# Kernel tuning notes

Measured on AMD Instinct MI355X. Metric: run time of the kernel, lower is better.

## Reference

```python
import jax, jax.numpy as jnp
import numpy as np

B, T, K, H = 8, 1024, 128, 8
TOP_K = 64
KS = 5  # conv kernel size for Q/K
DN = ('NCH', 'OIH', 'NCH')


def setup_inputs() -> dict:
    key = jax.random.key(0)
    ks = jax.random.split(key, 9)
    s = 0.05
    return {
        'x': jax.random.normal(ks[0], (B, T, K), jnp.float32),
        'Wq': jax.random.normal(ks[1], (K * H, K, KS), jnp.float32) * s,
        'bq': jax.random.normal(ks[2], (K * H,), jnp.float32) * s,
        'Wk': jax.random.normal(ks[3], (K * H, K, KS), jnp.float32) * s,
        'bk': jax.random.normal(ks[4], (K * H,), jnp.float32) * s,
        'Wv': jax.random.normal(ks[5], (K * H, K, 1), jnp.float32) * s,
        'bv': jax.random.normal(ks[6], (K * H,), jnp.float32) * s,
        'Wu': jax.random.normal(ks[7], (K, K * H), jnp.float32) * s,
        'bu': jax.random.normal(ks[8], (K,), jnp.float32) * s,
    }


def _prep(z, b, k, h, t, scale):
    # z: (b, k*h, t) conv output; torch view(b,k,h,t) then transposes -> (b,h,t,k)
    z = z.reshape(b, k, h, t)
    z = jnp.transpose(z, (0, 2, 3, 1)) * scale  # (b, h, t, k)
    # torch: transpose(1,2).contiguous().view(b*h, t, k) -- replicate exactly
    z = jnp.transpose(z, (0, 2, 1, 3)).reshape(b * h, t, k)
    return z


def reference(x, Wq, bq, Wk, bk, Wv, bv, Wu, bu):
    b, t, k = x.shape
    h = H
    xc = jnp.transpose(x, (0, 2, 1))  # (b, k, t)
    # causal left-pad KS-1 for Q/K convs; V is pointwise (kernel 1)
    q = jax.lax.conv_general_dilated(xc, Wq, (1,), [(KS - 1, 0)], dimension_numbers=DN) + bq[None, :, None]
    kk = jax.lax.conv_general_dilated(xc, Wk, (1,), [(KS - 1, 0)], dimension_numbers=DN) + bk[None, :, None]
    v = jax.lax.conv_general_dilated(xc, Wv, (1,), [(0, 0)], dimension_numbers=DN) + bv[None, :, None]
    scale = k ** -0.25
    q = _prep(q, b, k, h, t, scale)
    kk = _prep(kk, b, k, h, t, scale)
    v = _prep(v, b, k, h, t, 1.0)
    w = jnp.einsum('btk,bsk->bts', q, kk)  # (b*h, t, t)
    # top-k sparsification: keep entries >= k-th largest per row, else row min
    largest, _ = jax.lax.top_k(w, TOP_K)
    thresh = jnp.min(largest, axis=-1, keepdims=True)
    row_min = jnp.min(w, axis=-1, keepdims=True)
    w = jnp.where(w >= thresh, w, row_min)
    # causal mask (strict upper triangle -> -inf)
    causal = jnp.triu(jnp.ones((t, t), bool), 1)
    w = jnp.where(causal[None], -jnp.inf, w)
    w = jax.nn.softmax(w, axis=-1)
    out = jnp.einsum('bts,bsk->btk', w, v)  # (b*h, t, k)
    out = out.reshape(b, h, t, k)
    out = jnp.transpose(out, (0, 2, 1, 3)).reshape(b, t, k * h)
    return out @ Wu.T + bu
```

## Files before the change

### kernel.cpp

```cpp
#include <hip/hip_runtime.h>
#include <hip/hip_fp16.h>
#include <cstdint>

using f16 = _Float16;
typedef __attribute__((ext_vector_type(8))) _Float16 f16x8;
typedef __attribute__((ext_vector_type(4))) _Float16 f16x4;
typedef __attribute__((ext_vector_type(4))) float f32x4;

#define MFMA16(a, b, c) __builtin_amdgcn_mfma_f32_16x16x32_f16((a), (b), (c), 0, 0, 0)

__device__ __forceinline__ f16x8 ldfrag(const f16* p) { return *(const f16x8*)p; }

__device__ __forceinline__ void dma16(const f16* g, f16* l) {
  __builtin_amdgcn_global_load_lds(
      (const __attribute__((address_space(1))) void*)g,
      (__attribute__((address_space(3))) void*)l, 16, 0, 0);
}
__device__ __forceinline__ void wait_vm0() {
  asm volatile("s_waitcnt vmcnt(0)" ::: "memory");
}
__device__ __forceinline__ void wait_lgkm0() {
  asm volatile("s_waitcnt lgkmcnt(0)" ::: "memory");
}
__device__ __forceinline__ void wait_vm4() {
  asm volatile("s_waitcnt vmcnt(4)" ::: "memory");
}
__device__ __forceinline__ void wait_vm2() {
  asm volatile("s_waitcnt vmcnt(2)" ::: "memory");
}

static const int64_t NX = 1048576;
static const int64_t NW = 655360;
static const int64_t NV = 131072;

__global__ __launch_bounds__(256) void k0_prep(
    const float* __restrict__ x, const float* __restrict__ Wq,
    const float* __restrict__ Wk, const float* __restrict__ Wv,
    const float* __restrict__ Wu,
    f16* __restrict__ xh, f16* __restrict__ xl,
    f16* __restrict__ Wqh, f16* __restrict__ Wql,
    f16* __restrict__ Wkh, f16* __restrict__ Wkl,
    f16* __restrict__ Wvb, f16* __restrict__ Wub) {
  int64_t i = (int64_t)blockIdx.x * 256 + threadIdx.x;
  if (i < NX) {
    const float v = x[i];
    const f16 h = (f16)v;
    xh[i] = h; xl[i] = (f16)(v - (float)h);
  } else if (i < NX + NW) {
    int64_t d = i - NX;
    int j = (int)(d >> 17);
    int rem = (int)(d & 131071);
    int o = rem >> 7, c = rem & 127;
    const float v = Wq[(int64_t)(o * 128 + c) * 5 + j];
    const f16 h = (f16)v;
    Wqh[d] = h; Wql[d] = (f16)(v - (float)h);
  } else if (i < NX + 2 * NW) {
    int64_t d = i - NX - NW;
    int j = (int)(d >> 17);
    int rem = (int)(d & 131071);
    int o = rem >> 7, c = rem & 127;
    const float v = Wk[(int64_t)(o * 128 + c) * 5 + j];
    const f16 h = (f16)v;
    Wkh[d] = h; Wkl[d] = (f16)(v - (float)h);
  } else if (i < NX + 2 * NW + NV) {
    int64_t d = i - NX - 2 * NW;
    Wvb[d] = (f16)Wv[d];
  } else {
    int64_t d = i - NX - 2 * NW - NV;
    Wub[d] = (f16)Wu[d];
  }
}

#define STAGE_QK(DST, PASS, VALEXPR)                                    \
  {                                                                     \
    __syncthreads();                                                    \
    _Pragma("unroll")                                                   \
    for (int nt = 0; nt < 8; ++nt) {                                    \
      const int o = o0 + nt * 16 + lo;                                  \
      const int kcl = (o >> 3) & 63, hh = o & 7;                        \
      _Pragma("unroll")                                                 \
      for (int rtl = 0; rtl < 2; ++rtl) {                               \
        const int rt = (PASS) * 2 + rtl;                                \
        _Pragma("unroll")                                               \
        for (int r = 0; r < 4; ++r) {                                   \
          const int t2l = (rtl * 16 + quad * 4 + r) * 8 + hh;           \
          lds[t2l * 72 + kcl] = (VALEXPR);                              \
        }                                                               \
      }                                                                 \
    }                                                                   \
    __syncthreads();                                                    \
    _Pragma("unroll")                                                   \
    for (int p = 0; p < 8; ++p) {                                       \
      const int idx = p * 256 + tid;                                    \
      const int a = idx >> 3, c8 = (idx & 7) * 8;                       \
      *(f16x8*)(DST + ((int64_t)m * 1024 + t2b + (PASS) * 256 + a) * 128 + \
                half * 64 + c8) = *(const f16x8*)&lds[a * 72 + c8];     \
    }                                                                   \
  }

__global__ __launch_bounds__(256) void k1_conv(
    const f16* __restrict__ xh, const f16* __restrict__ xl,
    const f16* __restrict__ Wqh, const f16* __restrict__ Wql,
    const f16* __restrict__ Wkh, const f16* __restrict__ Wkl,
    const f16* __restrict__ Wvb,
    const float* __restrict__ bq, const float* __restrict__ bk,
    const float* __restrict__ bv,
    f16* __restrict__ q3h, f16* __restrict__ q3l,
    f16* __restrict__ k3h, f16* __restrict__ k3l,
    f16* __restrict__ v3T) {
  __shared__ f16 shm[36384];
  f16* const wbuf = shm;
  f16* const xbuf = shm + 18432;
  f16* const lds  = shm;
  const int tid = threadIdx.x;
  const int w = tid >> 6, lane = tid & 63;
  const int quad = lane >> 4, lo = lane & 15;
  const int r0 = blockIdx.x * 64;
  const int bb = r0 >> 10;
  const int m  = r0 >> 7;
  const int t2b = (r0 & 127) * 8;
  const int tloc = r0 & 1023;
  const int half = blockIdx.y;
  const int isK = blockIdx.z;
  const int o0 = half * 512 + w * 128;

  const f16* Wh = isK ? Wkh : Wqh;
  const f16* Wl = isK ? Wkl : Wql;
  const float* bias = isK ? bk : bq;

#pragma unroll
  for (int p = 0; p < 9; ++p) {
    const int u = p * 256 + tid;
    if (u < 2176) {
      const int row = u >> 5, tz = (u >> 4) & 1, c8 = (u & 15) * 8;
      int lt = tloc - 4 + row;
      if (lt < 0) lt = 0;
      const f16* src = (tz ? xl : xh) + ((int64_t)(bb * 1024 + lt)) * 128 + c8;
      *(f16x8*)&xbuf[row * 264 + tz * 128 + c8] = *(const f16x8*)src;
    }
  }
  __syncthreads();

  const int64_t wlane = (int64_t)(lane & 15) * 128 + (lane >> 4) * 8;

  if (!isK) {
    f32x4 av[4][8];
#pragma unroll
    for (int rt = 0; rt < 4; ++rt)
#pragma unroll
      for (int i = 0; i < 8; ++i)
#pragma unroll
        for (int r = 0; r < 4; ++r) av[rt][i][r] = 0.f;

#pragma unroll
    for (int g = 0; g < 4; ++g) {
#pragma unroll
      for (int s = 0; s < 2; ++s) {
        const int64_t vsrc = (int64_t)(o0 + (g * 2 + s) * 16) * 128 + wlane;
#pragma unroll
        for (int kk = 0; kk < 4; ++kk)
          dma16(Wvb + vsrc + kk * 32, wbuf + w * 4096 + s * 2048 + kk * 512);
      }
      wait_vm0();
#pragma unroll
      for (int kk = 0; kk < 4; ++kk) {
        f16x8 a[4];
#pragma unroll
        for (int rt = 0; rt < 4; ++rt)
          a[rt] = *(const f16x8*)&xbuf[(rt * 16 + lo + 4) * 264 + kk * 32 +
                                       quad * 8];
#pragma unroll
        for (int s = 0; s < 2; ++s) {
          const f16x8 bv8 = *(const f16x8*)&wbuf[w * 4096 + s * 2048 + kk * 512 +
                                                 quad * 128 + lo * 8];
#pragma unroll
          for (int rt = 0; rt < 4; ++rt)
            av[rt][g * 2 + s] = MFMA16(a[rt], bv8, av[rt][g * 2 + s]);
        }
      }
      wait_lgkm0();
    }
    __syncthreads();
#pragma unroll
    for (int pass = 0; pass < 2; ++pass) {
#pragma unroll
      for (int nt = 0; nt < 8; ++nt) {
        const int o = o0 + nt * 16 + lo;
        const float vbv = bv[o];
        const int kcl = (o >> 3) & 63, hh = o & 7;
#pragma unroll
        for (int rtl = 0; rtl < 2; ++rtl)
#pragma unroll
          for (int r = 0; r < 4; ++r) {
            const int t2l = (rtl * 16 + quad * 4 + r) * 8 + hh;
            lds[kcl * 264 + t2l] = (f16)(av[pass * 2 + rtl][nt][r] + vbv);
          }
      }
      __syncthreads();
#pragma unroll
      for (int p = 0; p < 8; ++p) {
        const int idx = p * 256 + tid;
        const int kcl = idx >> 5, t8 = (idx & 31) * 8;
        *(f16x8*)(v3T + ((int64_t)m * 128 + half * 64 + kcl) * 1024 + t2b +
                  pass * 256 + t8) = *(const f16x8*)&lds[kcl * 264 + t8];
      }
      __syncthreads();
    }
  }

  f32x4 aq[4][8];
#pragma unroll
  for (int rt = 0; rt < 4; ++rt)
#pragma unroll
    for (int i = 0; i < 8; ++i)
#pragma unroll
      for (int r = 0; r < 4; ++r) { aq[rt][i][r] = 0.f; }

  for (int j = 0; j < 5; ++j) {
    const bool z0 = (tloc == 0);
#pragma unroll
    for (int kk = 0; kk < 4; ++kk) {
      f16x8 ah[4], al[4];
#pragma unroll
      for (int rt = 0; rt < 4; ++rt) {
        ah[rt] = *(const f16x8*)&xbuf[(rt * 16 + lo + j) * 264 + kk * 32 +
                                      quad * 8];
        al[rt] = *(const f16x8*)&xbuf[(rt * 16 + lo + j) * 264 + 128 + kk * 32 +
                                      quad * 8];
      }
      if (z0 && (lo + j < 4)) {
#pragma unroll
        for (int e = 0; e < 8; ++e) { ah[0][e] = (f16)0; al[0][e] = (f16)0; }
      }
#pragma unroll
      for (int ntg = 0; ntg < 2; ++ntg) {
        const int64_t wsrc = (int64_t)j * 131072 + kk * 32 + wlane;
#pragma unroll
        for (int ntl = 0; ntl < 4; ++ntl) {
          const int nt = ntg * 4 + ntl;
          const int64_t o = wsrc + (int64_t)(o0 + nt * 16) * 128;
          dma16(Wh + o, wbuf + w * 4096 + ntl * 1024);
          dma16(Wl + o, wbuf + w * 4096 + ntl * 1024 + 512);
        }
        wait_vm4();
#pragma unroll
        for (int ntl = 0; ntl < 4; ++ntl) {
          if (ntl == 2) wait_vm0();
          const int nt = ntg * 4 + ntl;
          const f16x8 bh = *(const f16x8*)&wbuf[w * 4096 + ntl * 1024 +
                                                quad * 128 + lo * 8];
          const f16x8 bl = *(const f16x8*)&wbuf[w * 4096 + ntl * 1024 + 512 +
                                                quad * 128 + lo * 8];
#pragma unroll
          for (int rt = 0; rt < 4; ++rt) {
            aq[rt][nt] = MFMA16(ah[rt], bh, aq[rt][nt]);
            aq[rt][nt] = MFMA16(ah[rt], bl, aq[rt][nt]);
            aq[rt][nt] = MFMA16(al[rt], bh, aq[rt][nt]);
          }
        }
        wait_lgkm0();
      }
    }
  }

  const float SC = 0.29730177875068026f;
#pragma unroll
  for (int nt = 0; nt < 8; ++nt) {
    const int o = o0 + nt * 16 + lo;
    const float vb = bias[o];
#pragma unroll
    for (int rt = 0; rt < 4; ++rt)
#pragma unroll
      for (int r = 0; r < 4; ++r) aq[rt][nt][r] = (aq[rt][nt][r] + vb) * SC;
  }

  if (!isK) {
    STAGE_QK(q3h, 0, (f16)aq[rt][nt][r])
    STAGE_QK(q3h, 1, (f16)aq[rt][nt][r])
    STAGE_QK(q3l, 0, (f16)(aq[rt][nt][r] - (float)(f16)aq[rt][nt][r]))
    STAGE_QK(q3l, 1, (f16)(aq[rt][nt][r] - (float)(f16)aq[rt][nt][r]))
  } else {
    STAGE_QK(k3h, 0, (f16)aq[rt][nt][r])
    STAGE_QK(k3h, 1, (f16)aq[rt][nt][r])
    STAGE_QK(k3l, 0, (f16)(aq[rt][nt][r] - (float)(f16)aq[rt][nt][r]))
    STAGE_QK(k3l, 1, (f16)(aq[rt][nt][r] - (float)(f16)aq[rt][nt][r]))
  }
}

__global__ __launch_bounds__(512, 4) void k234_attn(
    const f16* __restrict__ q3h, const f16* __restrict__ q3l,
    const f16* __restrict__ k3h, const f16* __restrict__ k3l,
    const f16* __restrict__ v3T, f16* __restrict__ A) {
  __shared__ float Sb[16 * 516];
  __shared__ f16 kbuf[16384];
  const int tid = threadIdx.x;
  const int w = tid >> 6, lane = tid & 63;
  const int quad = lane >> 4, lo = lane & 15;
  const int qd = lane & 3, cit = lane >> 2;
  const int qsw = qd ^ ((cit >> 1) & 3);
  const int fro = (lo * 4 + (quad ^ ((lo >> 1) & 3))) * 8;
  const int hid = blockIdx.y * 64 + blockIdx.x;
  const int m = (hid & 7) * 8 + ((hid >> 3) >> 6);
  const int r0 = ((hid >> 3) & 63) * 16;

  const int64_t qoff = ((int64_t)m * 1024 + r0 + lo) * 128;
  f16x8 qh[4], ql[4];
#pragma unroll
  for (int kk = 0; kk < 4; ++kk) {
    qh[kk] = ldfrag(q3h + qoff + kk * 32 + quad * 8);
    ql[kk] = ldfrag(q3l + qoff + kk * 32 + quad * 8);
  }

  unsigned key[2][16];
  unsigned kmn0 = 0xFFFFFFFFu, kmn1 = 0xFFFFFFFFu;

#pragma unroll
  for (int half = 0; half < 2; ++half) {
    f32x4 acc[4];
#pragma unroll
    for (int i = 0; i < 4; ++i)
#pragma unroll
      for (int r = 0; r < 4; ++r) acc[i][r] = 0.f;

    for (int kp = 0; kp < 2; ++kp) {
#pragma unroll
      for (int cc = 0; cc < 4; ++cc) {
        const int c0 = half * 512 + cc * 128;
        const int64_t rowg = (int64_t)(m * 1024 + c0 + w * 16 + cit) * 128;
#pragma unroll
        for (int t = 0; t < 2; ++t) {
          const f16* srcb = t ? k3l : k3h;
#pragma unroll
          for (int kkh = 0; kkh < 2; ++kkh)
            dma16(srcb + rowg + (kp * 2 + kkh) * 32 + qsw * 8,
                  kbuf + (w * 4 + t * 2 + kkh) * 512);
        }
        wait_vm0();
#pragma unroll
        for (int kkh = 0; kkh < 2; ++kkh) {
          const int kkg = kp * 2 + kkh;
          f16x8 bh = *(const f16x8*)(kbuf + (w * 4 + kkh) * 512 + fro);
          f16x8 bl = *(const f16x8*)(kbuf + (w * 4 + 2 + kkh) * 512 + fro);
          acc[cc] = MFMA16(qh[kkg], bh, acc[cc]);
          acc[cc] = MFMA16(qh[kkg], bl, acc[cc]);
          acc[cc] = MFMA16(ql[kkg], bh, acc[cc]);
        }
        wait_lgkm0();
      }
    }
#pragma unroll
    for (int cc = 0; cc < 4; ++cc)
#pragma unroll
      for (int r = 0; r < 4; ++r)
        Sb[(quad * 4 + r) * 516 + cc * 128 + w * 16 + lo] = acc[cc][r];
    __syncthreads();
#pragma unroll
    for (int rr = 0; rr < 2; ++rr) {
      const float4* rp = (const float4*)(Sb + (w * 2 + rr) * 516);
#pragma unroll
      for (int i2 = 0; i2 < 2; ++i2) {
        const float4 f4 = rp[i2 * 64 + lane];
        const float fe[4] = {f4.x, f4.y, f4.z, f4.w};
#pragma unroll
        for (int e = 0; e < 4; ++e) {
          const unsigned u = __builtin_bit_cast(unsigned, fe[e]);
          const unsigned k = (u & 0x80000000u) ? ~u : (u | 0x80000000u);
          key[rr][half * 8 + i2 * 4 + e] = k;
          if (rr == 0) kmn0 = min(kmn0, k); else kmn1 = min(kmn1, k);
        }
      }
    }
    __syncthreads();
  }

  const int64_t vrow = (int64_t)(m * 128 + w * 16 + cit) * 1024;
  const int nkb = (r0 >> 6) + 1;
#define VISSUE(KB, PAIR)                                                 \
  {                                                                      \
    dma16(v3T + vrow + (KB) * 64 + qsw * 8,                              \
          kbuf + (w * 4 + (PAIR) * 2) * 512);                            \
    dma16(v3T + vrow + (KB) * 64 + 32 + qsw * 8,                         \
          kbuf + (w * 4 + (PAIR) * 2 + 1) * 512);                        \
  }
  VISSUE(0, 0)
  if (nkb > 1) VISSUE(1, 1)

  f16* P16 = (f16*)Sb;
  {
#pragma unroll
    for (int off = 32; off; off >>= 1) {
      kmn0 = min(kmn0, (unsigned)__shfl_xor((int)kmn0, off));
      kmn1 = min(kmn1, (unsigned)__shfl_xor((int)kmn1, off));
    }
    unsigned th0 = 0u, th1 = 0u;
    bool d0 = false, d1 = false;
    for (int b = 31; b >= 0; --b) {
      if (!d0) {
        const unsigned c0 = th0 | (1u << b);
        int cnt0 = 0;
#pragma unroll
        for (int i = 0; i < 16; ++i)
          cnt0 += (int)__popcll(__ballot(key[0][i] >= c0));
        if (cnt0 >= 64) { th0 = c0; if (cnt0 == 64) d0 = true; }
      }
      if (!d1) {
        const unsigned c1 = th1 | (1u << b);
        int cnt1 = 0;
#pragma unroll
        for (int i = 0; i < 16; ++i)
          cnt1 += (int)__popcll(__ballot(key[1][i] >= c1));
        if (cnt1 >= 64) { th1 = c1; if (cnt1 == 64) d1 = true; }
      }
      if (d0 && d1) break;
    }

#pragma unroll
    for (int rr = 0; rr < 2; ++rr) {
      const unsigned kth = rr ? th1 : th0;
      const unsigned kmn = rr ? kmn1 : kmn0;
      const int row = w * 2 + rr, t2 = r0 + row;
      const unsigned umn = (kmn & 0x80000000u) ? (kmn ^ 0x80000000u) : ~kmn;
      const float mn = __builtin_bit_cast(float, umn);
      const unsigned ukv = (kth & 0x80000000u) ? (kth ^ 0x80000000u) : ~kth;
      const float kv = __builtin_bit_cast(float, ukv);

      float ev[16];
      float sum = 0.f;
#pragma unroll
      for (int j = 0; j < 16; ++j) {
        const int s = (j >> 3) * 512 + ((j >> 2) & 1) * 256 + lane * 4 + (j & 3);
        const unsigned k = key[rr][j];
        const unsigned uu = (k & 0x80000000u) ? (k ^ 0x80000000u) : ~k;
        const float f = __builtin_bit_cast(float, uu);
        const float ww = (k >= kth) ? f : mn;
        const float x = (s <= t2) ? __expf(ww - kv) : 0.f;
        ev[j] = x;
        sum += x;
      }
      for (int off = 32; off; off >>= 1) sum += __shfl_xor(sum, off);
      const float inv = 1.0f / sum;

      f16* prow = P16 + row * 1032;
#pragma unroll
      for (int hh = 0; hh < 2; ++hh)
#pragma unroll
        for (int i2 = 0; i2 < 2; ++i2) {
          f16x4 pk;
#pragma unroll
          for (int e = 0; e < 4; ++e)
            pk[e] = (f16)(ev[hh * 8 + i2 * 4 + e] * inv);
          *(f16x4*)(prow + hh * 512 + i2 * 256 + lane * 4) = pk;
        }
    }
  }
  __syncthreads();

  {
    f32x4 oa0, oa1;
#pragma unroll
    for (int r = 0; r < 4; ++r) { oa0[r] = 0.f; oa1[r] = 0.f; }
    for (int kb = 0; kb < nkb; ++kb) {
      if (kb + 1 < nkb) wait_vm2();
      else wait_vm0();
      const int pair = kb & 1;
      {
        const f16x8 vf0 = *(const f16x8*)(kbuf + (w * 4 + pair * 2) * 512 + fro);
        const f16x8 vf1 =
            *(const f16x8*)(kbuf + (w * 4 + pair * 2 + 1) * 512 + fro);
        const f16x8 af0 = *(const f16x8*)(P16 + lo * 1032 + kb * 64 + quad * 8);
        const f16x8 af1 =
            *(const f16x8*)(P16 + lo * 1032 + kb * 64 + 32 + quad * 8);
        oa0 = MFMA16(af0, vf0, oa0);
        oa1 = MFMA16(af1, vf1, oa1);
      }
      wait_lgkm0();
      if (kb + 2 < nkb) VISSUE(kb + 2, pair)
    }
#undef VISSUE
#pragma unroll
    for (int r = 0; r < 4; ++r)
      A[((int64_t)m * 1024 + r0 + quad * 4 + r) * 128 + w * 16 + lo] =
          (f16)(oa0[r] + oa1[r]);
  }
}

__global__ __launch_bounds__(256) void k5_proj(
    const f16* __restrict__ A, const f16* __restrict__ Wub,
    const float* __restrict__ bu, float* __restrict__ out) {
  const int w = threadIdx.x >> 6, lane = threadIdx.x & 63;
  const int quad = lane >> 4, lo = lane & 15;
  const int rt = w & 1, ch = w >> 1;
  const int r0 = blockIdx.x * 32 + rt * 16;
  const int r = r0 + lo;
  const int bI = r >> 10, t2 = r & 1023;

  f32x4 acc[4];
#pragma unroll
  for (int i = 0; i < 4; ++i)
#pragma unroll
    for (int rr = 0; rr < 4; ++rr) acc[i][rr] = 0.f;

#pragma unroll 2
  for (int kk = 0; kk < 32; ++kk) {
    const int o = kk * 32 + quad * 8;
    const int j = o >> 7, kc = o & 127;
    f16x8 a = ldfrag(A + (((int64_t)(bI * 8 + j) * 1024 + t2) * 128 + kc));
    f16x8 wb[4];
#pragma unroll
    for (int nt = 0; nt < 4; ++nt)
      wb[nt] = ldfrag(Wub + (int64_t)(ch * 64 + nt * 16 + lo) * 1024 + o);
#pragma unroll
    for (int nt = 0; nt < 4; ++nt) acc[nt] = MFMA16(a, wb[nt], acc[nt]);
  }
#pragma unroll
  for (int nt = 0; nt < 4; ++nt) {
    const int col = ch * 64 + nt * 16 + lo;
    const float bias = bu[col];
#pragma unroll
    for (int rr = 0; rr < 4; ++rr) {
      const int row = r0 + quad * 4 + rr;
      out[(int64_t)row * 128 + col] = acc[nt][rr] + bias;
    }
  }
}

extern "C" void kernel_launch(void* const* d_in, const int* in_sizes, int n_in,
                              void* d_out, int out_size, void* d_ws, size_t ws_size,
                              hipStream_t stream) {
  const float* x  = (const float*)d_in[0];
  const float* Wq = (const float*)d_in[1];
  const float* bq = (const float*)d_in[2];
  const float* Wk = (const float*)d_in[3];
  const float* bk = (const float*)d_in[4];
  const float* Wv = (const float*)d_in[5];
  const float* bv = (const float*)d_in[6];
  const float* Wu = (const float*)d_in[7];
  const float* bu = (const float*)d_in[8];
  float* out = (float*)d_out;

  char* ws = (char*)d_ws;
  f16* xh  = (f16*)ws;  ws += 2097152;
  f16* xl  = (f16*)ws;  ws += 2097152;
  f16* Wqh = (f16*)ws;  ws += 1310720;
  f16* Wql = (f16*)ws;  ws += 1310720;
  f16* Wkh = (f16*)ws;  ws += 1310720;
  f16* Wkl = (f16*)ws;  ws += 1310720;
  f16* Wvb = (f16*)ws;  ws += 262144;
  f16* Wub = (f16*)ws;  ws += 262144;
  f16* q3h = (f16*)ws;  ws += 16777216;
  f16* q3l = (f16*)ws;  ws += 16777216;
  f16* k3h = (f16*)ws;  ws += 16777216;
  f16* k3l = (f16*)ws;  ws += 16777216;
  f16* v3T = (f16*)ws;  ws += 16777216;
  f16* A   = (f16*)ws;  ws += 16777216;

  k0_prep<<<10240, 256, 0, stream>>>(x, Wq, Wk, Wv, Wu,
                                     xh, xl, Wqh, Wql, Wkh, Wkl, Wvb, Wub);

  k1_conv<<<dim3(128, 2, 2), 256, 0, stream>>>(xh, xl, Wqh, Wql, Wkh, Wkl, Wvb,
                                               bq, bk, bv, q3h, q3l, k3h, k3l,
                                               v3T);

  k234_attn<<<dim3(64, 64), 512, 0, stream>>>(q3h, q3l, k3h, k3l, v3T, A);

  k5_proj<<<256, 256, 0, stream>>>(A, Wub, bu, out);

  (void)in_sizes; (void)n_in; (void)out_size; (void)ws_size;
}
```

Baseline: 411.7 us.

## Software-pipeline weight DMA in Q/K conv loop with half-chunk prefetch

Restructures the Q/K conv projection loop so the global-to-LDS weight loads for the next chunk are issued in two halves while the current chunk's MFMAs run. Each half's buffer slot is refilled right after its MFMAs read it, and waits are tuned with vmcnt. This hides weight-load latency that was previously exposed, since each chunk waited for its own DMA. It adds prologue issues and more intricate waitcnt logic, where a wrong count could cause races.

```diff
diff --git a/kernel.cpp b/kernel.cpp
--- a/kernel.cpp
+++ b/kernel.cpp
@@ -216,52 +216,88 @@
 #pragma unroll
       for (int r = 0; r < 4; ++r) { aq[rt][i][r] = 0.f; }
 
+  const int64_t wbase = wlane + (int64_t)o0 * 128;
+#define ISSUE_HALF(J, KK, NTG, H)                                       \
+  {                                                                     \
+    _Pragma("unroll")                                                   \
+    for (int ntl2 = 0; ntl2 < 2; ++ntl2) {                              \
+      const int ntl_ = (H) * 2 + ntl2;                                  \
+      const int64_t o_ = wbase + (int64_t)(J) * 131072 + (KK) * 32 +    \
+                         (int64_t)(((NTG) * 4 + ntl_) * 16) * 128;      \
+      dma16(Wh + o_, wbuf + w * 4096 + ntl_ * 1024);                    \
+      dma16(Wl + o_, wbuf + w * 4096 + ntl_ * 1024 + 512);              \
+    }                                                                   \
+  }
+
+  ISSUE_HALF(0, 0, 0, 0)
+  ISSUE_HALF(0, 0, 0, 1)
+
+  const bool z0 = (tloc == 0);
   for (int j = 0; j < 5; ++j) {
-    const bool z0 = (tloc == 0);
-#pragma unroll
-    for (int kk = 0; kk < 4; ++kk) {
-      f16x8 ah[4], al[4];
-#pragma unroll
-      for (int rt = 0; rt < 4; ++rt) {
-        ah[rt] = *(const f16x8*)&xbuf[(rt * 16 + lo + j) * 264 + kk * 32 +
-                                      quad * 8];
-        al[rt] = *(const f16x8*)&xbuf[(rt * 16 + lo + j) * 264 + 128 + kk * 32 +
-                                      quad * 8];
-      }
-      if (z0 && (lo + j < 4)) {
-#pragma unroll
-        for (int e = 0; e < 8; ++e) { ah[0][e] = (f16)0; al[0][e] = (f16)0; }
-      }
-#pragma unroll
-      for (int ntg = 0; ntg < 2; ++ntg) {
-        const int64_t wsrc = (int64_t)j * 131072 + kk * 32 + wlane;
-#pragma unroll
-        for (int ntl = 0; ntl < 4; ++ntl) {
-          const int nt = ntg * 4 + ntl;
-          const int64_t o = wsrc + (int64_t)(o0 + nt * 16) * 128;
-          dma16(Wh + o, wbuf + w * 4096 + ntl * 1024);
-          dma16(Wl + o, wbuf + w * 4096 + ntl * 1024 + 512);
-        }
+    f16x8 ah[4], al[4];
+#pragma unroll
+    for (int c = 0; c < 8; ++c) {
+      const int kk = c >> 1, ntg = c & 1;
+      if (ntg == 0) {
+#pragma unroll
+        for (int rt = 0; rt < 4; ++rt) {
+          ah[rt] = *(const f16x8*)&xbuf[(rt * 16 + lo + j) * 264 + kk * 32 +
+                                        quad * 8];
+          al[rt] = *(const f16x8*)&xbuf[(rt * 16 + lo + j) * 264 + 128 +
+                                        kk * 32 + quad * 8];
+        }
+        if (z0 && (lo + j < 4)) {
+#pragma unroll
+          for (int e = 0; e < 8; ++e) { ah[0][e] = (f16)0; al[0][e] = (f16)0; }
+        }
+      }
+      const int nj = (c == 7) ? j + 1 : j;
+      const int nkk = (c == 7) ? 0 : ((c + 1) >> 1);
+      const int nntg = (c == 7) ? 0 : ((c + 1) & 1);
+      const bool more = (c < 7) || (j < 4);
+
+      wait_vm4();
+#pragma unroll
+      for (int ntl = 0; ntl < 2; ++ntl) {
+        const int nt = ntg * 4 + ntl;
+        const f16x8 bh = *(const f16x8*)&wbuf[w * 4096 + ntl * 1024 +
+                                              quad * 128 + lo * 8];
+        const f16x8 bl = *(const f16x8*)&wbuf[w * 4096 + ntl * 1024 + 512 +
+                                              quad * 128 + lo * 8];
+#pragma unroll
+        for (int rt = 0; rt < 4; ++rt) {
+          aq[rt][nt] = MFMA16(ah[rt], bh, aq[rt][nt]);
+          aq[rt][nt] = MFMA16(ah[rt], bl, aq[rt][nt]);
+          aq[rt][nt] = MFMA16(al[rt], bh, aq[rt][nt]);
+        }
+      }
+      wait_lgkm0();
+      if (more) ISSUE_HALF(nj, nkk, nntg, 0)
+
+      if (c == 7) {
+        if (j == 4) wait_vm0(); else wait_vm4();
+      } else {
         wait_vm4();
-#pragma unroll
-        for (int ntl = 0; ntl < 4; ++ntl) {
-          if (ntl == 2) wait_vm0();
-          const int nt = ntg * 4 + ntl;
-          const f16x8 bh = *(const f16x8*)&wbuf[w * 4096 + ntl * 1024 +
-                                                quad * 128 + lo * 8];
-          const f16x8 bl = *(const f16x8*)&wbuf[w * 4096 + ntl * 1024 + 512 +
-                                                quad * 128 + lo * 8];
-#pragma unroll
-          for (int rt = 0; rt < 4; ++rt) {
-            aq[rt][nt] = MFMA16(ah[rt], bh, aq[rt][nt]);
-            aq[rt][nt] = MFMA16(ah[rt], bl, aq[rt][nt]);
-            aq[rt][nt] = MFMA16(al[rt], bh, aq[rt][nt]);
-          }
-        }
-        wait_lgkm0();
-      }
-    }
-  }
+      }
+#pragma unroll
+      for (int ntl = 2; ntl < 4; ++ntl) {
+        const int nt = ntg * 4 + ntl;
+        const f16x8 bh = *(const f16x8*)&wbuf[w * 4096 + ntl * 1024 +
+                                              quad * 128 + lo * 8];
+        const f16x8 bl = *(const f16x8*)&wbuf[w * 4096 + ntl * 1024 + 512 +
+                                              quad * 128 + lo * 8];
+#pragma unroll
+        for (int rt = 0; rt < 4; ++rt) {
+          aq[rt][nt] = MFMA16(ah[rt], bh, aq[rt][nt]);
+          aq[rt][nt] = MFMA16(ah[rt], bl, aq[rt][nt]);
+          aq[rt][nt] = MFMA16(al[rt], bh, aq[rt][nt]);
+        }
+      }
+      wait_lgkm0();
+      if (more) ISSUE_HALF(nj, nkk, nntg, 1)
+    }
+  }
+#undef ISSUE_HALF
 
   const float SC = 0.29730177875068026f;
 #pragma unroll
```

Result: no change. 408.2 us (-0.9%).
